# Kernel optimization log

Measured on AMD Instinct MI355X. Metric: run time of the kernel, lower is better.

## Reference

```python
import jax, jax.numpy as jnp
import numpy as np
from math import sqrt

B, S, D = 4, 2048, 1024


def setup_inputs() -> dict:
    key = jax.random.key(0)
    k1, k2, k3, k4 = jax.random.split(key, 4)
    scale = 1.0 / sqrt(D)  # roughly nn.Linear init magnitude
    x = jax.random.normal(k1, (B, S, D), dtype=jnp.float32)
    Wq = jax.random.normal(k2, (D, D), dtype=jnp.float32) * scale
    Wk = jax.random.normal(k3, (D, D), dtype=jnp.float32) * scale
    Wv = jax.random.normal(k4, (D, D), dtype=jnp.float32) * scale
    attn_mask = jnp.ones((B, S), dtype=jnp.int32)  # 1 = attend, 0 = pad
    return {"x": x, "attn_mask": attn_mask, "Wq": Wq, "Wk": Wk, "Wv": Wv}


def reference(x, attn_mask, Wq, Wk, Wv):
    # torch nn.Linear: y = x @ W.T (no bias)
    q = jnp.einsum("bsd,ed->bse", x, Wq)
    k = jnp.einsum("bsd,ed->bse", x, Wk)
    v = jnp.einsum("bsd,ed->bse", x, Wv)

    scores = jnp.einsum("bqd,bkd->bqk", q, k)  # [B, S, S]

    # causal mask (upper triangle above diagonal masked out)
    causal_mask = jnp.triu(jnp.ones((S, S), dtype=bool), k=1)  # [S, S]
    scores = jnp.where(causal_mask[None, :, :], -jnp.inf, scores)

    # padding mask: attn_mask [B, S] broadcast over query dim
    pad = (attn_mask == 0)[:, None, :]  # [B, 1, S]
    scores = jnp.where(pad, -jnp.inf, scores)

    attn_weights = jax.nn.softmax(scores / sqrt(D), axis=-1)
    return jnp.einsum("bqk,bkd->bqd", attn_weights, v)
```

## Files before the change

### kernel.cpp

```cpp
#include <hip/hip_runtime.h>
#include <stdint.h>
#include <math.h>

#define BK 64
#define LSTR 64
#define ETS 132
#define TSH 8192
#define TSH32 4096

typedef __attribute__((ext_vector_type(8))) short short8;
typedef __attribute__((ext_vector_type(16))) float floatx16;

typedef __attribute__((address_space(3))) unsigned int lds_u32;
typedef const __attribute__((address_space(1))) unsigned int glb_u32;

__device__ __forceinline__ unsigned short f2bf(float f) {
    union { float f; unsigned u; } x; x.f = f;
    unsigned r = x.u + 0x7fffu + ((x.u >> 16) & 1u);
    return (unsigned short)(r >> 16);
}

__global__ void cvt_kernel(const float* __restrict__ x,
                           const float* __restrict__ wq,
                           const float* __restrict__ wk,
                           const float* __restrict__ wv,
                           unsigned short* __restrict__ xb,
                           unsigned short* __restrict__ wb,
                           float* __restrict__ lsum) {
    int i4 = (blockIdx.x * 256 + threadIdx.x) * 4;
    if (blockIdx.x < 8) {
        float4 z = (float4){0.f, 0.f, 0.f, 0.f};
        *(float4*)(lsum + i4) = z;
    }
    const float* src; unsigned short* dst; int off;
    if (i4 < 8388608)       { src = x;  dst = xb;            off = i4; }
    else if (i4 < 9437184)  { src = wq; dst = wb;            off = i4 - 8388608; }
    else if (i4 < 10485760) { src = wk; dst = wb + 1048576;  off = i4 - 9437184; }
    else                    { src = wv; dst = wb + 2097152;  off = i4 - 10485760; }
    float4 v = *(const float4*)(src + off);
    ushort4 o;
    o.x = f2bf(v.x); o.y = f2bf(v.y); o.z = f2bf(v.z); o.w = f2bf(v.w);
    *(ushort4*)(dst + off) = o;
}

__device__ __forceinline__ void stage_async(unsigned short* sh, const unsigned short* g,
                                            int ld, int tid) {
#pragma unroll
    for (int it = 0; it < 4; ++it) {
        int c = it * 256 + tid;
        int row = c >> 3, cc = c & 7;
        int gcc = cc ^ (row & 7);
        __builtin_amdgcn_global_load_lds(
            (glb_u32*)(g + (size_t)row * ld + gcc * 8),
            (lds_u32*)(sh + c * 8), 16, 0, 0);
    }
}

__device__ __forceinline__ void mfma_step(const unsigned short* Ash, const unsigned short* Bsh,
                                          int lane, int wr, int wc, floatx16 acc[2][2]) {
    int lm = lane & 31, lg = lane >> 5;
#pragma unroll
    for (int h = 0; h < 4; ++h) {
        short8 af[2], bf[2];
#pragma unroll
        for (int i = 0; i < 2; ++i) {
            int ar = wr * 64 + i * 32 + lm;
            int br = wc * 64 + i * 32 + lm;
            af[i] = *(const short8*)(Ash + ar * LSTR + (((h << 1) | lg) ^ (ar & 7)) * 8);
            bf[i] = *(const short8*)(Bsh + br * LSTR + (((h << 1) | lg) ^ (br & 7)) * 8);
        }
#pragma unroll
        for (int i = 0; i < 2; ++i)
#pragma unroll
            for (int j = 0; j < 2; ++j)
                acc[i][j] = __builtin_amdgcn_mfma_f32_32x32x16_bf16(af[i], bf[j], acc[i][j], 0, 0, 0);
    }
}

__device__ __forceinline__ void stage_async32(unsigned short* sh, const unsigned short* g,
                                              int ld, int tid) {
#pragma unroll
    for (int it = 0; it < 2; ++it) {
        int c = it * 256 + tid;
        int row = c >> 2, cc = c & 3;
        int gcc = cc ^ ((row >> 1) & 3);
        __builtin_amdgcn_global_load_lds(
            (glb_u32*)(g + (size_t)row * ld + gcc * 8),
            (lds_u32*)(sh + c * 8), 16, 0, 0);
    }
}

__device__ __forceinline__ void mfma_step32(const unsigned short* Ash, const unsigned short* Bsh,
                                            int lane, int wr, int wc, floatx16 acc[2][2]) {
    int lm = lane & 31, lg = lane >> 5;
#pragma unroll
    for (int h = 0; h < 2; ++h) {
        short8 af[2], bf[2];
#pragma unroll
        for (int i = 0; i < 2; ++i) {
            int ar = wr * 64 + i * 32 + lm;
            int br = wc * 64 + i * 32 + lm;
            af[i] = *(const short8*)(Ash + ar * 32 + ((((h << 1) | lg) ^ ((ar >> 1) & 3)) * 8));
            bf[i] = *(const short8*)(Bsh + br * 32 + ((((h << 1) | lg) ^ ((br >> 1) & 3)) * 8));
        }
#pragma unroll
        for (int i = 0; i < 2; ++i)
#pragma unroll
            for (int j = 0; j < 2; ++j)
                acc[i][j] = __builtin_amdgcn_mfma_f32_32x32x16_bf16(af[i], bf[j], acc[i][j], 0, 0, 0);
    }
}

#define ACC_ZERO {0.f,0.f,0.f,0.f,0.f,0.f,0.f,0.f,0.f,0.f,0.f,0.f,0.f,0.f,0.f,0.f}


__global__ __launch_bounds__(256) void qkv_gemm(const unsigned short* __restrict__ Xb,
                                                const unsigned short* __restrict__ Wb,
                                                unsigned short* __restrict__ Qb,
                                                unsigned short* __restrict__ Kb,
                                                unsigned short* __restrict__ Vt) {
    __shared__ unsigned short shbuf[4 * TSH];
    int tid = threadIdx.x;
    int bm = blockIdx.x, bn = blockIdx.y;
    int lane = tid & 63, w = tid >> 6, wr = w >> 1, wc = w & 1;
    floatx16 acc[2][2] = {{ACC_ZERO, ACC_ZERO}, {ACC_ZERO, ACC_ZERO}};

    const unsigned short* Ag = Xb + (size_t)bm * 128 * 1024;
    const unsigned short* Bg = Wb + (size_t)bn * 128 * 1024;
    stage_async(shbuf, Ag, 1024, tid);
    stage_async(shbuf + 2 * TSH, Bg, 1024, tid);
    __syncthreads();
#pragma unroll 2
    for (int t = 0; t < 16; ++t) {
        int cur = t & 1;
        unsigned short* Ash = shbuf + cur * TSH;
        unsigned short* Bsh = shbuf + (2 + cur) * TSH;
        if (t < 15) {
            stage_async(shbuf + (cur ^ 1) * TSH, Ag + (t + 1) * BK, 1024, tid);
            stage_async(shbuf + (2 + (cur ^ 1)) * TSH, Bg + (t + 1) * BK, 1024, tid);
        }
        mfma_step(Ash, Bsh, lane, wr, wc, acc);
        __syncthreads();
    }

    int which = bn >> 3;
    int nnb = (bn & 7) * 128;
    int lm = lane & 31, lg = lane >> 5;
    if (which < 2) {
#pragma unroll
        for (int i = 0; i < 2; ++i)
#pragma unroll
            for (int j = 0; j < 2; ++j)
#pragma unroll
                for (int p = 0; p < 16; ++p) {
                    int row = wr * 64 + i * 32 + (p & 3) + 8 * (p >> 2) + 4 * lg;
                    shbuf[row * ETS + wc * 64 + j * 32 + lm] = f2bf(acc[i][j][p]);
                }
    } else {
#pragma unroll
        for (int i = 0; i < 2; ++i)
#pragma unroll
            for (int j = 0; j < 2; ++j)
#pragma unroll
                for (int g = 0; g < 4; ++g) {
                    int mb = wr * 64 + i * 32 + 8 * g + 4 * lg;
                    ushort4 o;
                    o.x = f2bf(acc[i][j][4 * g + 0]); o.y = f2bf(acc[i][j][4 * g + 1]);
                    o.z = f2bf(acc[i][j][4 * g + 2]); o.w = f2bf(acc[i][j][4 * g + 3]);
                    *(ushort4*)(shbuf + (wc * 64 + j * 32 + lm) * ETS + mb) = o;
                }
    }
    __syncthreads();

    unsigned short* gbase; size_t gld;
    if (which == 0)      { gbase = Qb + (size_t)(bm * 128) * 1024 + nnb; gld = 1024; }
    else if (which == 1) { gbase = Kb + (size_t)(bm * 128) * 1024 + nnb; gld = 1024; }
    else { gbase = Vt + ((size_t)(bm >> 4) * 1024 + nnb) * 2048 + (bm & 15) * 128; gld = 2048; }
#pragma unroll
    for (int it = 0; it < 4; ++it) {
        int row = it * 32 + (tid >> 3), cc = tid & 7;
        uint4 v0 = *(const uint4*)(shbuf + row * ETS + cc * 8);
        uint4 v1 = *(const uint4*)(shbuf + row * ETS + 64 + cc * 8);
        *(uint4*)(gbase + (size_t)row * gld + cc * 8) = v0;
        *(uint4*)(gbase + (size_t)row * gld + 64 + cc * 8) = v1;
    }
}

__global__ __launch_bounds__(256) void scores_gemm(const unsigned short* __restrict__ Qb,
                                                   const unsigned short* __restrict__ Kb,
                                                   const int* __restrict__ mask,
                                                   unsigned short* __restrict__ Pb,
                                                   float* __restrict__ lsum) {
    int u = blockIdx.x, b = blockIdx.y;
    int ti = (int)((sqrtf(8.0f * (float)u + 1.0f) - 1.0f) * 0.5f);
    while ((ti + 1) * (ti + 2) / 2 <= u) ti++;
    while (ti * (ti + 1) / 2 > u) ti--;
    int tj = u - ti * (ti + 1) / 2;

    __shared__ unsigned short shbuf[128 * ETS];
    int tid = threadIdx.x;
    int lane = tid & 63, w = tid >> 6, wr = w >> 1, wc = w & 1;
    floatx16 acc[2][2] = {{ACC_ZERO, ACC_ZERO}, {ACC_ZERO, ACC_ZERO}};

    const unsigned short* Ag = Qb + ((size_t)b * 2048 + ti * 128) * 1024;
    const unsigned short* Bg = Kb + ((size_t)b * 2048 + tj * 128) * 1024;
    stage_async32(shbuf, Ag, 1024, tid);
    stage_async32(shbuf + 2 * TSH32, Bg, 1024, tid);
    __syncthreads();
#pragma unroll 2
    for (int t = 0; t < 32; ++t) {
        int cur = t & 1;
        unsigned short* Ash = shbuf + cur * TSH32;
        unsigned short* Bsh = shbuf + (2 + cur) * TSH32;
        if (t < 31) {
            stage_async32(shbuf + (cur ^ 1) * TSH32, Ag + (t + 1) * 32, 1024, tid);
            stage_async32(shbuf + (2 + (cur ^ 1)) * TSH32, Bg + (t + 1) * 32, 1024, tid);
        }
        mfma_step32(Ash, Bsh, lane, wr, wc, acc);
        __syncthreads();
    }

    int lm = lane & 31, lg = lane >> 5;
    int mk[2];
#pragma unroll
    for (int j = 0; j < 2; ++j)
        mk[j] = mask[b * 2048 + tj * 128 + wc * 64 + j * 32 + lm];

    float* lrow_sum = lsum + b * 2048;
#pragma unroll
    for (int i = 0; i < 2; ++i) {
#pragma unroll
        for (int p = 0; p < 16; ++p) {
            int rloc = wr * 64 + i * 32 + (p & 3) + 8 * (p >> 2) + 4 * lg;
            int q = ti * 128 + rloc;
            float rs = 0.f;
#pragma unroll
            for (int j = 0; j < 2; ++j) {
                int n = tj * 128 + wc * 64 + j * 32 + lm;
                float pv = 0.f;
                if (n <= q && mk[j] != 0) pv = __expf(acc[i][j][p] * 0.03125f);
                rs += pv;
                shbuf[rloc * ETS + wc * 64 + j * 32 + lm] = f2bf(pv);
            }
#pragma unroll
            for (int o = 1; o <= 16; o <<= 1) rs += __shfl_xor(rs, o);
            if (lm == 0) atomicAdd(&lrow_sum[q], rs);
        }
    }
    __syncthreads();

    unsigned short* gbase = Pb + ((size_t)b * 2048 + ti * 128) * 2048 + tj * 128;
#pragma unroll
    for (int it = 0; it < 4; ++it) {
        int row = it * 32 + (tid >> 3), cc = tid & 7;
        uint4 v0 = *(const uint4*)(shbuf + row * ETS + cc * 8);
        uint4 v1 = *(const uint4*)(shbuf + row * ETS + 64 + cc * 8);
        *(uint4*)(gbase + (size_t)row * 2048 + cc * 8) = v0;
        *(uint4*)(gbase + (size_t)row * 2048 + 64 + cc * 8) = v1;
    }
}

__global__ __launch_bounds__(256) void pv_gemm(const unsigned short* __restrict__ Pb,
                                               const unsigned short* __restrict__ Vt,
                                               const float* __restrict__ lsum,
                                               float* __restrict__ out) {
    int bid = blockIdx.x;
    int half = bid >> 8, rr = bid & 255;
    int tig = rr >> 5;
    int ti = half ? tig : 15 - tig;
    int dj = (rr >> 2) & 7;
    int b  = rr & 3;
    __shared__ unsigned short shbuf[4 * TSH];
    int tid = threadIdx.x;
    int lane = tid & 63, w = tid >> 6, wr = w >> 1, wc = w & 1;
    floatx16 acc[2][2] = {{ACC_ZERO, ACC_ZERO}, {ACC_ZERO, ACC_ZERO}};

    const unsigned short* Ag = Pb + ((size_t)b * 2048 + ti * 128) * 2048;
    const unsigned short* Bg = Vt + ((size_t)b * 1024 + dj * 128) * 2048;
    int nt = (ti + 1) * 2;
    stage_async(shbuf, Ag, 2048, tid);
    stage_async(shbuf + 2 * TSH, Bg, 2048, tid);
    __syncthreads();
    for (int t = 0; t < nt; ++t) {
        int cur = t & 1;
        unsigned short* Ash = shbuf + cur * TSH;
        unsigned short* Bsh = shbuf + (2 + cur) * TSH;
        if (t + 1 < nt) {
            stage_async(shbuf + (cur ^ 1) * TSH, Ag + (t + 1) * BK, 2048, tid);
            stage_async(shbuf + (2 + (cur ^ 1)) * TSH, Bg + (t + 1) * BK, 2048, tid);
        }
        mfma_step(Ash, Bsh, lane, wr, wc, acc);
        __syncthreads();
    }

    int lm = lane & 31, lg = lane >> 5;
#pragma unroll
    for (int i = 0; i < 2; ++i) {
#pragma unroll
        for (int g = 0; g < 4; ++g) {
            int qb = ti * 128 + wr * 64 + i * 32 + 8 * g + 4 * lg;
#pragma unroll
            for (int r = 0; r < 4; ++r) {
                float invl = 1.f / lsum[b * 2048 + qb + r];
#pragma unroll
                for (int j = 0; j < 2; ++j) {
                    int d = dj * 128 + wc * 64 + j * 32 + lm;
                    out[((size_t)b * 2048 + qb + r) * 1024 + d] = acc[i][j][4 * g + r] * invl;
                }
            }
        }
    }
}

extern "C" void kernel_launch(void* const* d_in, const int* in_sizes, int n_in,
                              void* d_out, int out_size, void* d_ws, size_t ws_size,
                              hipStream_t stream) {
    const float* x    = (const float*)d_in[0];
    const int*   mask = (const int*)d_in[1];
    const float* wq   = (const float*)d_in[2];
    const float* wk   = (const float*)d_in[3];
    const float* wv   = (const float*)d_in[4];
    float* out = (float*)d_out;
    char* ws = (char*)d_ws;

    unsigned short* Xb = (unsigned short*)(ws + 0);
    unsigned short* Wb = (unsigned short*)(ws + 16777216);
    unsigned short* Qb = (unsigned short*)(ws + 23068672);
    unsigned short* Kb = (unsigned short*)(ws + 39845888);
    unsigned short* Vt = (unsigned short*)(ws + 56623104);
    unsigned short* Pb = (unsigned short*)(ws + 73400320);
    float*        lsum = (float*)(ws + 106954752);
    (void)ws_size; (void)in_sizes; (void)n_in; (void)out_size;

    cvt_kernel<<<11264, 256, 0, stream>>>(x, wq, wk, wv, Xb, Wb, lsum);
    qkv_gemm<<<dim3(64, 24), 256, 0, stream>>>(Xb, Wb, Qb, Kb, Vt);
    scores_gemm<<<dim3(136, 4), 256, 0, stream>>>(Qb, Kb, mask, Pb, lsum);
    pv_gemm<<<512, 256, 0, stream>>>(Pb, Vt, lsum, out);
}
```

Measured before the change: 224.0 us.

## Widen QKV GEMM tile to 128x256 with BK=32 double buffering

The QKV projection GEMM now computes a 128x256 output tile per block instead of 128x128. Each wave owns all 128 rows and 64 columns, accumulating 4x2 MFMA tiles. The K step shrinks to 32 so the LDS footprint stays small, and launch bounds ask for 3 blocks per CU. The epilogue writes the tile back in two 128-column halves through the shared buffer. The aim is more reuse of the A operand and more MFMA work per LDS load, at the cost of more accumulator registers, twice as many K-loop iterations and syncs, and half as many blocks in the grid.

```diff
diff --git a/kernel.cpp b/kernel.cpp
--- a/kernel.cpp
+++ b/kernel.cpp
@@ -7,6 +7,7 @@
 #define ETS 132
 #define TSH 8192
 #define TSH32 4096
+#define TBH32 8192
 
 typedef __attribute__((ext_vector_type(8))) short short8;
 typedef __attribute__((ext_vector_type(16))) float floatx16;
@@ -90,6 +91,19 @@
     }
 }
 
+__device__ __forceinline__ void stage_async32b(unsigned short* sh, const unsigned short* g,
+                                               int ld, int tid) {
+#pragma unroll
+    for (int it = 0; it < 4; ++it) {
+        int c = it * 256 + tid;
+        int row = c >> 2, cc = c & 3;
+        int gcc = cc ^ ((row >> 1) & 3);
+        __builtin_amdgcn_global_load_lds(
+            (glb_u32*)(g + (size_t)row * ld + gcc * 8),
+            (lds_u32*)(sh + c * 8), 16, 0, 0);
+    }
+}
+
 __device__ __forceinline__ void mfma_step32(const unsigned short* Ash, const unsigned short* Bsh,
                                             int lane, int wr, int wc, floatx16 acc[2][2]) {
     int lm = lane & 31, lg = lane >> 5;
@@ -114,75 +128,115 @@
 #define ACC_ZERO {0.f,0.f,0.f,0.f,0.f,0.f,0.f,0.f,0.f,0.f,0.f,0.f,0.f,0.f,0.f,0.f}
 
 
-__global__ __launch_bounds__(256) void qkv_gemm(const unsigned short* __restrict__ Xb,
-                                                const unsigned short* __restrict__ Wb,
-                                                unsigned short* __restrict__ Qb,
-                                                unsigned short* __restrict__ Kb,
-                                                unsigned short* __restrict__ Vt) {
-    __shared__ unsigned short shbuf[4 * TSH];
+__global__ __launch_bounds__(256, 3) void qkv_gemm(const unsigned short* __restrict__ Xb,
+                                                   const unsigned short* __restrict__ Wb,
+                                                   unsigned short* __restrict__ Qb,
+                                                   unsigned short* __restrict__ Kb,
+                                                   unsigned short* __restrict__ Vt) {
+    __shared__ unsigned short shbuf[2 * TSH32 + 2 * TBH32];
     int tid = threadIdx.x;
     int bm = blockIdx.x, bn = blockIdx.y;
-    int lane = tid & 63, w = tid >> 6, wr = w >> 1, wc = w & 1;
-    floatx16 acc[2][2] = {{ACC_ZERO, ACC_ZERO}, {ACC_ZERO, ACC_ZERO}};
+    int lane = tid & 63, wn = tid >> 6;
+    int lm = lane & 31, lg = lane >> 5;
+    floatx16 acc[4][2];
+#pragma unroll
+    for (int mi = 0; mi < 4; ++mi)
+#pragma unroll
+        for (int nj = 0; nj < 2; ++nj)
+            acc[mi][nj] = (floatx16)0.f;
 
     const unsigned short* Ag = Xb + (size_t)bm * 128 * 1024;
-    const unsigned short* Bg = Wb + (size_t)bn * 128 * 1024;
-    stage_async(shbuf, Ag, 1024, tid);
-    stage_async(shbuf + 2 * TSH, Bg, 1024, tid);
+    const unsigned short* Bg = Wb + (size_t)bn * 256 * 1024;
+    stage_async32 (shbuf, Ag, 1024, tid);
+    stage_async32b(shbuf + 2 * TSH32, Bg, 1024, tid);
     __syncthreads();
-#pragma unroll 2
-    for (int t = 0; t < 16; ++t) {
+    for (int t = 0; t < 32; ++t) {
         int cur = t & 1;
-        unsigned short* Ash = shbuf + cur * TSH;
-        unsigned short* Bsh = shbuf + (2 + cur) * TSH;
-        if (t < 15) {
-            stage_async(shbuf + (cur ^ 1) * TSH, Ag + (t + 1) * BK, 1024, tid);
-            stage_async(shbuf + (2 + (cur ^ 1)) * TSH, Bg + (t + 1) * BK, 1024, tid);
-        }
-        mfma_step(Ash, Bsh, lane, wr, wc, acc);
+        const unsigned short* Ash = shbuf + cur * TSH32;
+        const unsigned short* Bsh = shbuf + 2 * TSH32 + cur * TBH32;
+        if (t < 31) {
+            stage_async32 (shbuf + (cur ^ 1) * TSH32, Ag + (t + 1) * 32, 1024, tid);
+            stage_async32b(shbuf + 2 * TSH32 + (cur ^ 1) * TBH32, Bg + (t + 1) * 32, 1024, tid);
+        }
+#pragma unroll
+        for (int h = 0; h < 2; ++h) {
+            short8 af[4], bf[2];
+#pragma unroll
+            for (int mi = 0; mi < 4; ++mi) {
+                int ar = mi * 32 + lm;
+                af[mi] = *(const short8*)(Ash + ar * 32 + ((((h << 1) | lg) ^ ((ar >> 1) & 3)) * 8));
+            }
+#pragma unroll
+            for (int nj = 0; nj < 2; ++nj) {
+                int br = wn * 64 + nj * 32 + lm;
+                bf[nj] = *(const short8*)(Bsh + br * 32 + ((((h << 1) | lg) ^ ((br >> 1) & 3)) * 8));
+            }
+#pragma unroll
+            for (int mi = 0; mi < 4; ++mi)
+#pragma unroll
+                for (int nj = 0; nj < 2; ++nj)
+                    acc[mi][nj] = __builtin_amdgcn_mfma_f32_32x32x16_bf16(af[mi], bf[nj], acc[mi][nj], 0, 0, 0);
+        }
         __syncthreads();
     }
 
-    int which = bn >> 3;
-    int nnb = (bn & 7) * 128;
-    int lm = lane & 31, lg = lane >> 5;
+    int which = bn >> 2;
+    int nnb = (bn & 3) * 256;
     if (which < 2) {
-#pragma unroll
-        for (int i = 0; i < 2; ++i)
-#pragma unroll
-            for (int j = 0; j < 2; ++j)
-#pragma unroll
-                for (int p = 0; p < 16; ++p) {
-                    int row = wr * 64 + i * 32 + (p & 3) + 8 * (p >> 2) + 4 * lg;
-                    shbuf[row * ETS + wc * 64 + j * 32 + lm] = f2bf(acc[i][j][p]);
-                }
+        unsigned short* gq = (which == 0 ? Qb : Kb) + (size_t)(bm * 128) * 1024 + nnb;
+#pragma unroll
+        for (int c = 0; c < 2; ++c) {
+            __syncthreads();
+            if ((wn >> 1) == c) {
+                int colb = (wn & 1) * 64;
+#pragma unroll
+                for (int mi = 0; mi < 4; ++mi)
+#pragma unroll
+                    for (int nj = 0; nj < 2; ++nj)
+#pragma unroll
+                        for (int p = 0; p < 16; ++p) {
+                            int row = mi * 32 + (p & 3) + 8 * (p >> 2) + 4 * lg;
+                            shbuf[row * ETS + colb + nj * 32 + lm] = f2bf(acc[mi][nj][p]);
+                        }
+            }
+            __syncthreads();
+#pragma unroll
+            for (int it = 0; it < 8; ++it) {
+                int row = it * 16 + (tid >> 4), cg = tid & 15;
+                *(uint4*)(gq + (size_t)row * 1024 + c * 128 + cg * 8) =
+                    *(const uint4*)(shbuf + row * ETS + cg * 8);
+            }
+        }
     } else {
 #pragma unroll
-        for (int i = 0; i < 2; ++i)
-#pragma unroll
-            for (int j = 0; j < 2; ++j)
-#pragma unroll
-                for (int g = 0; g < 4; ++g) {
-                    int mb = wr * 64 + i * 32 + 8 * g + 4 * lg;
-                    ushort4 o;
-                    o.x = f2bf(acc[i][j][4 * g + 0]); o.y = f2bf(acc[i][j][4 * g + 1]);
-                    o.z = f2bf(acc[i][j][4 * g + 2]); o.w = f2bf(acc[i][j][4 * g + 3]);
-                    *(ushort4*)(shbuf + (wc * 64 + j * 32 + lm) * ETS + mb) = o;
-                }
-    }
-    __syncthreads();
-
-    unsigned short* gbase; size_t gld;
-    if (which == 0)      { gbase = Qb + (size_t)(bm * 128) * 1024 + nnb; gld = 1024; }
-    else if (which == 1) { gbase = Kb + (size_t)(bm * 128) * 1024 + nnb; gld = 1024; }
-    else { gbase = Vt + ((size_t)(bm >> 4) * 1024 + nnb) * 2048 + (bm & 15) * 128; gld = 2048; }
-#pragma unroll
-    for (int it = 0; it < 4; ++it) {
-        int row = it * 32 + (tid >> 3), cc = tid & 7;
-        uint4 v0 = *(const uint4*)(shbuf + row * ETS + cc * 8);
-        uint4 v1 = *(const uint4*)(shbuf + row * ETS + 64 + cc * 8);
-        *(uint4*)(gbase + (size_t)row * gld + cc * 8) = v0;
-        *(uint4*)(gbase + (size_t)row * gld + 64 + cc * 8) = v1;
+        for (int c = 0; c < 2; ++c) {
+            __syncthreads();
+            if ((wn >> 1) == c) {
+#pragma unroll
+                for (int mi = 0; mi < 4; ++mi)
+#pragma unroll
+                    for (int nj = 0; nj < 2; ++nj) {
+                        int noff = (wn & 1) * 64 + nj * 32 + lm;
+#pragma unroll
+                        for (int g = 0; g < 4; ++g) {
+                            int m = mi * 32 + 8 * g + 4 * lg;
+                            ushort4 o;
+                            o.x = f2bf(acc[mi][nj][4 * g + 0]); o.y = f2bf(acc[mi][nj][4 * g + 1]);
+                            o.z = f2bf(acc[mi][nj][4 * g + 2]); o.w = f2bf(acc[mi][nj][4 * g + 3]);
+                            *(ushort4*)(shbuf + noff * ETS + m) = o;
+                        }
+                    }
+            }
+            __syncthreads();
+            unsigned short* gv = Vt + ((size_t)(bm >> 4) * 1024 + nnb + c * 128) * 2048
+                                 + (bm & 15) * 128;
+#pragma unroll
+            for (int it = 0; it < 8; ++it) {
+                int n = it * 16 + (tid >> 4), mg = tid & 15;
+                *(uint4*)(gv + (size_t)n * 2048 + mg * 8) =
+                    *(const uint4*)(shbuf + n * ETS + mg * 8);
+            }
+        }
     }
 }
 
@@ -333,7 +387,7 @@
     (void)ws_size; (void)in_sizes; (void)n_in; (void)out_size;
 
     cvt_kernel<<<11264, 256, 0, stream>>>(x, wq, wk, wv, Xb, Wb, lsum);
-    qkv_gemm<<<dim3(64, 24), 256, 0, stream>>>(Xb, Wb, Qb, Kb, Vt);
+    qkv_gemm<<<dim3(64, 12), 256, 0, stream>>>(Xb, Wb, Qb, Kb, Vt);
     scores_gemm<<<dim3(136, 4), 256, 0, stream>>>(Qb, Kb, mask, Pb, lsum);
     pv_gemm<<<512, 256, 0, stream>>>(Pb, Vt, lsum, out);
 }
```

After: 226.0 us. About the same (+0.9%).
